# Optimization experiments

Measured on AMD Instinct MI355X. Metric: run time of the kernel, lower is better.

Reference implementation:

```python
import jax, jax.numpy as jnp
import numpy as np

C = 256      # in/out channels
PSI = 4
W = C // PSI          # window width = 64
D = W // 2            # stride = 32
HEADS = 2 * PSI - 1   # 7


def conv_bn_relu(x, Wmat, scale, bias):
    # 1x1 conv (no bias) + inference-mode BN (folded to per-channel scale/bias) + ReLU
    y = jnp.einsum('oc,bcn->bon', Wmat, x)
    return jax.nn.relu(y * scale[:, None] + bias[:, None])


def setup_inputs() -> dict:
    key = jax.random.key(0)
    ks = jax.random.split(key, 16)
    B, N = 4, 2048
    x = jax.random.normal(ks[0], (B, C, N), dtype=jnp.float32)
    Wq = jax.random.normal(ks[1], (C, C), dtype=jnp.float32) / np.sqrt(C)
    Wk = jax.random.normal(ks[2], (C, C), dtype=jnp.float32) / np.sqrt(C)
    Wv = jax.random.normal(ks[3], (C, C), dtype=jnp.float32) / np.sqrt(C)
    sq = jax.random.uniform(ks[4], (C,), dtype=jnp.float32, minval=0.5, maxval=1.5)
    bq = jax.random.normal(ks[5], (C,), dtype=jnp.float32) * 0.1
    sk = jax.random.uniform(ks[6], (C,), dtype=jnp.float32, minval=0.5, maxval=1.5)
    bk = jax.random.normal(ks[7], (C,), dtype=jnp.float32) * 0.1
    sv = jax.random.uniform(ks[8], (C,), dtype=jnp.float32, minval=0.5, maxval=1.5)
    bv = jax.random.normal(ks[9], (C,), dtype=jnp.float32) * 0.1
    Wf = jax.random.normal(ks[10], (C, HEADS * W), dtype=jnp.float32) / np.sqrt(HEADS * W)
    bf = jax.random.normal(ks[11], (C,), dtype=jnp.float32) * 0.1
    sf = jax.random.uniform(ks[12], (C,), dtype=jnp.float32, minval=0.5, maxval=1.5)
    bff = jax.random.normal(ks[13], (C,), dtype=jnp.float32) * 0.1
    return dict(x=x, Wq=Wq, sq=sq, bq=bq, Wk=Wk, sk=sk, bk=bk,
                Wv=Wv, sv=sv, bv=bv, Wf=Wf, bf=bf, sf=sf, bff=bff)


def reference(x, Wq, sq, bq, Wk, sk, bk, Wv, sv, bv, Wf, bf, sf, bff):
    q = conv_bn_relu(x, Wq, sq, bq)   # [B, C, N]
    k = conv_bn_relu(x, Wk, sk, bk)
    v = conv_bn_relu(x, Wv, sv, bv)

    # overlapping channel windows: head m covers channels [m*D, m*D+W)
    win = jnp.arange(HEADS)[:, None] * D + jnp.arange(W)[None, :]  # [HEADS, W]
    qw = q[:, win, :]  # [B, HEADS, W, N]
    kw = k[:, win, :]
    vw = v[:, win, :]

    # a_m = q_m^T k_m over channel window -> [B, HEADS, N, N]
    attn = jnp.einsum('bhwn,bhwm->bhnm', qw, kw)
    attn = jax.nn.softmax(attn, axis=-1)
    # o_m = (a_m v_m^T)^T -> [B, HEADS, W, N]
    o = jnp.einsum('bhnm,bhwm->bhwn', attn, vw)

    B, _, _, N = o.shape
    O = o.reshape(B, HEADS * W, N)  # concat heads along channel dim

    # fusion: 1x1 conv (with bias) + BN + ReLU
    y = jnp.einsum('oc,bcn->bon', Wf, O) + bf[:, None]
    return jax.nn.relu(y * sf[:, None] + bff[:, None])
```

## Files before the change

kernel.cpp:

```cpp
#include <hip/hip_runtime.h>
#include <hip/hip_bf16.h>

typedef __attribute__((ext_vector_type(8))) short bf16x8;
typedef __attribute__((ext_vector_type(4))) float f32x4;

namespace {
constexpr int kC = 256;
constexpr int kN = 2048;
constexpr int kB = 4;
constexpr int kHeads = 7;
constexpr int kOC = kHeads * 64;
constexpr int kSplit = 2;
constexpr int kMChunk = kN / kSplit;
constexpr float kLog2e = 1.44269504f;
}

static __device__ __forceinline__ float bf2f(ushort u) {
    union { unsigned u; float f; } v; v.u = ((unsigned)u) << 16;
    return v.f;
}
static __device__ __forceinline__ unsigned pk_bf16(float a, float b) {
    __hip_bfloat162 h = __float22bfloat162_rn(make_float2(a, b));
    union { __hip_bfloat162 h; unsigned u; } v; v.h = h;
    return v.u;
}
static __device__ __forceinline__ ushort f2bf(float f) {
    return (ushort)(pk_bf16(f, 0.f) & 0xffffu);
}
static __device__ __forceinline__ ushort4 pack4bf(float a, float b, float c, float d) {
    union { ushort4 s; uint2 u; } v;
    v.u.x = pk_bf16(a, b); v.u.y = pk_bf16(c, d);
    return v.s;
}
static __device__ __forceinline__ float fexp2(float x) {
#if __has_builtin(__builtin_amdgcn_exp2f)
    return __builtin_amdgcn_exp2f(x);
#else
    return exp2f(x);
#endif
}
static __device__ __forceinline__ void g2l16(const ushort* g, ushort* l) {
    __builtin_amdgcn_global_load_lds(
        (const __attribute__((address_space(1))) void*)g,
        (__attribute__((address_space(3))) void*)l,
        16, 0, 0);
}

__global__ __launch_bounds__(256) void cast_w_kernel(
    const float* __restrict__ Wq, const float* __restrict__ Wk,
    const float* __restrict__ Wv, const float* __restrict__ Wf,
    ushort* __restrict__ wq, ushort* __restrict__ wk,
    ushort* __restrict__ wv, ushort* __restrict__ wf)
{
    int which = blockIdx.y;
    const float* src = which == 0 ? Wq : which == 1 ? Wk : which == 2 ? Wv : Wf;
    ushort* dst      = which == 0 ? wq : which == 1 ? wk : which == 2 ? wv : wf;
    int n = (which == 3) ? kC * kOC : kC * kC;
    int i = (blockIdx.x * 256 + threadIdx.x) * 4;
    if (i < n) {
        float4 v = *(const float4*)(src + i);
        *(ushort4*)(dst + i) = pack4bf(v.x, v.y, v.z, v.w);
    }
}

__global__ __launch_bounds__(256) void transpose_kernel(
    const float* __restrict__ x, ushort* __restrict__ xT)
{
    const int nt = blockIdx.x, ct = blockIdx.y, b = blockIdx.z;
    __shared__ float T[64][65];
    const int tid = threadIdx.x;
    const float* xb = x + ((size_t)b * kC + ct * 64) * kN + nt * 64;
#pragma unroll
    for (int p = 0; p < 16; ++p) {
        int idx = p * 256 + tid;
        int cc = idx >> 6, nn = idx & 63;
        T[cc][nn] = xb[(size_t)cc * kN + nn];
    }
    __syncthreads();
    ushort* xTb = xT + ((size_t)b * kN + nt * 64) * kC + ct * 64;
#pragma unroll
    for (int p = 0; p < 4; ++p) {
        int nn = p * 16 + (tid >> 4);
        int c4 = (tid & 15) * 4;
        *(ushort4*)&xTb[(size_t)nn * kC + c4] =
            pack4bf(T[c4 + 0][nn], T[c4 + 1][nn], T[c4 + 2][nn], T[c4 + 3][nn]);
    }
}

__global__ __launch_bounds__(256, 2) void qkv_kernel(
    const ushort* __restrict__ xT,
    const ushort* __restrict__ Wqb, const ushort* __restrict__ Wkb, const ushort* __restrict__ Wvb,
    const float* __restrict__ sq, const float* __restrict__ bq,
    const float* __restrict__ sk, const float* __restrict__ bk,
    const float* __restrict__ sv, const float* __restrict__ bv,
    ushort* __restrict__ qT, ushort* __restrict__ kT, ushort* __restrict__ vB)
{
    const int nt  = blockIdx.x;
    const int ot  = blockIdx.y;
    const int b   = blockIdx.z / 3;
    const int mat = blockIdx.z % 3;
    const ushort* Wb = mat == 0 ? Wqb : mat == 1 ? Wkb : Wvb;
    const float* sm = mat == 0 ? sq : mat == 1 ? sk : sv;
    const float* bm = mat == 0 ? bq : mat == 1 ? bk : bv;

    __shared__ __align__(16) ushort lds[4][128 * 64];

    const int tid = threadIdx.x;
    const int lane = tid & 63, wav = tid >> 6;
    const int quad = lane >> 4, l16 = lane & 15;

    const ushort* xTb = xT + ((size_t)b * kN + nt * 128) * kC;
    const ushort* Wt  = Wb + (size_t)(ot * 128) * kC;

    f32x4 acc[8][2];
#pragma unroll
    for (int mt = 0; mt < 8; ++mt)
#pragma unroll
        for (int ntt = 0; ntt < 2; ++ntt)
#pragma unroll
            for (int r = 0; r < 4; ++r) acc[mt][ntt][r] = 0.f;

    const int sa   = lane >> 3;
    const int sblk = (lane & 7) ^ sa;
    auto dmaK = [&](int k0, int buf) {
#pragma unroll
        for (int p = 0; p < 4; ++p) {
            int row = wav * 32 + p * 8 + sa;
            size_t so = (size_t)row * kC + k0 + sblk * 8;
            int dbase = (wav * 32 + p * 8) * 64;
            g2l16(Wt + so,  &lds[buf][dbase]);
            g2l16(xTb + so, &lds[2 + buf][dbase]);
        }
    };

    dmaK(0, 0);
    __syncthreads();

    for (int kt = 0; kt < 4; ++kt) {
        const int cur = kt & 1;
        const bool more = (kt < 3);
        if (more) dmaK((kt + 1) * 64, cur ^ 1);

        const ushort* rowB = (mat < 2) ? lds[cur] : lds[2 + cur];
        const ushort* colB = (mat < 2) ? lds[2 + cur] : lds[cur];
#pragma unroll
        for (int ks = 0; ks < 2; ++ks) {
            bf16x8 bfr[2];
#pragma unroll
            for (int ntt = 0; ntt < 2; ++ntt) {
                int row = wav * 32 + ntt * 16 + l16;
                bfr[ntt] = *(const bf16x8*)&colB[row * 64 + (((ks * 4 + quad) ^ (row & 7)) * 8)];
            }
#pragma unroll
            for (int mt = 0; mt < 8; ++mt) {
                int row = mt * 16 + l16;
                bf16x8 af = *(const bf16x8*)&rowB[row * 64 + (((ks * 4 + quad) ^ (row & 7)) * 8)];
#pragma unroll
                for (int ntt = 0; ntt < 2; ++ntt)
                    acc[mt][ntt] = __builtin_amdgcn_mfma_f32_16x16x32_bf16(
                        af, bfr[ntt], acc[mt][ntt], 0, 0, 0);
            }
        }
        __syncthreads();
    }

    ushort* sT = &lds[0][0];
    const float qs = (mat == 0) ? kLog2e : 1.f;

    if (mat < 2) {
#pragma unroll
        for (int mt = 0; mt < 8; ++mt) {
            float4 sc4 = *(const float4*)&sm[ot * 128 + mt * 16 + quad * 4];
            float4 bi4 = *(const float4*)&bm[ot * 128 + mt * 16 + quad * 4];
#pragma unroll
            for (int ntt = 0; ntt < 2; ++ntt) {
                int nrow = wav * 32 + ntt * 16 + l16;
                float v0 = fmaf(acc[mt][ntt][0], sc4.x, bi4.x) * qs;
                float v1 = fmaf(acc[mt][ntt][1], sc4.y, bi4.y) * qs;
                float v2 = fmaf(acc[mt][ntt][2], sc4.z, bi4.z) * qs;
                float v3 = fmaf(acc[mt][ntt][3], sc4.w, bi4.w) * qs;
                int cb = (mt * 2 + (quad >> 1)) ^ (nrow & 15);
                *(ushort4*)&sT[nrow * 128 + cb * 8 + (quad & 1) * 4] =
                    pack4bf(v0 > 0.f ? v0 : 0.f, v1 > 0.f ? v1 : 0.f,
                            v2 > 0.f ? v2 : 0.f, v3 > 0.f ? v3 : 0.f);
            }
        }
        __syncthreads();
        ushort* out = (mat == 0) ? qT : kT;
#pragma unroll
        for (int p = 0; p < 8; ++p) {
            int idx = p * 256 + tid;
            int row = idx >> 4, blk = idx & 15;
            int4 d = *(const int4*)&sT[row * 128 + ((blk ^ (row & 15)) * 8)];
            *(int4*)&out[((size_t)b * kN + nt * 128 + row) * kC + ot * 128 + blk * 8] = d;
        }
    } else {
#pragma unroll
        for (int ntt = 0; ntt < 2; ++ntt) {
            int orow = wav * 32 + ntt * 16 + l16;
            float sc = sm[ot * 128 + orow], bi = bm[ot * 128 + orow];
#pragma unroll
            for (int mt = 0; mt < 8; ++mt) {
                float v0 = fmaf(acc[mt][ntt][0], sc, bi);
                float v1 = fmaf(acc[mt][ntt][1], sc, bi);
                float v2 = fmaf(acc[mt][ntt][2], sc, bi);
                float v3 = fmaf(acc[mt][ntt][3], sc, bi);
                int cb = (mt * 2 + (quad >> 1)) ^ (orow & 15);
                *(ushort4*)&sT[orow * 128 + cb * 8 + (quad & 1) * 4] =
                    pack4bf(v0 > 0.f ? v0 : 0.f, v1 > 0.f ? v1 : 0.f,
                            v2 > 0.f ? v2 : 0.f, v3 > 0.f ? v3 : 0.f);
            }
        }
        __syncthreads();
#pragma unroll
        for (int p = 0; p < 8; ++p) {
            int idx = p * 256 + tid;
            int row = idx >> 4, blk = idx & 15;
            int4 d = *(const int4*)&sT[row * 128 + ((blk ^ (row & 15)) * 8)];
            *(int4*)&vB[((size_t)b * kC + ot * 128 + row) * kN + nt * 128 + blk * 8] = d;
        }
    }
}

__global__ __launch_bounds__(256, 3) void attn_kernel(
    const ushort* __restrict__ qT, const ushort* __restrict__ kT,
    const ushort* __restrict__ vB,
    ushort* __restrict__ Opart, float* __restrict__ Ls)
{
    const int n0 = blockIdx.x * 128;
    const int h  = blockIdx.y;
    const int s  = blockIdx.z & 1;
    const int b  = blockIdx.z >> 1;
    const int tid = threadIdx.x;
    const int lane = tid & 63, wav = tid >> 6;
    const int quad = lane >> 4, l16 = lane & 15;

    __shared__ __align__(16) ushort sKV[2][8192];
    __shared__ __align__(16) ushort sP[128 * 64];

    const ushort* qTb = qT + (size_t)b * kN * kC;
    const ushort* kTb = kT + (size_t)b * kN * kC;
    const ushort* vbb = vB + ((size_t)b * kC + h * 32) * kN;

    const int arr   = wav >> 1;
    const int rbase = (wav & 1) * 32;

    bf16x8 qf[2][2];
#pragma unroll
    for (int kk = 0; kk < 2; ++kk)
#pragma unroll
        for (int nt2 = 0; nt2 < 2; ++nt2) {
            int ng = n0 + wav * 32 + nt2 * 16 + l16;
            qf[kk][nt2] = *(const bf16x8*)(qTb + (size_t)ng * kC + h * 32 + kk * 32 + quad * 8);
        }

    f32x4 oacc[4][2];
#pragma unroll
    for (int wt = 0; wt < 4; ++wt)
#pragma unroll
        for (int nt2 = 0; nt2 < 2; ++nt2)
#pragma unroll
            for (int r = 0; r < 4; ++r) oacc[wt][nt2][r] = 0.f;
    float li[2] = {0.f, 0.f};

    const int mstart = s * kMChunk;
    const int NIT = kMChunk / 64;

    const int sa   = lane >> 3;
    const int sblk = (lane & 7) ^ sa;
    auto dmaTile = [&](int m0, int buf) {
#pragma unroll
        for (int p = 0; p < 4; ++p) {
            int rl = rbase + p * 8 + sa;
            const ushort* src = (arr == 0)
                ? (kTb + (size_t)(m0 + rl) * kC + h * 32 + sblk * 8)
                : (vbb + (size_t)rl * kN + m0 + sblk * 8);
            g2l16(src, &sKV[buf][arr * 4096 + (rbase + p * 8) * 64]);
        }
    };

    dmaTile(mstart, 0);
    __syncthreads();

    for (int it = 0; it < NIT; ++it) {
        const int cur = it & 1;
        const bool more = (it + 1 < NIT);
        if (more) dmaTile(mstart + (it + 1) * 64, cur ^ 1);

        const ushort* sK = &sKV[cur][0];
        const ushort* sV = &sKV[cur][4096];

        f32x4 sacc[4][2];
#pragma unroll
        for (int mt = 0; mt < 4; ++mt)
#pragma unroll
            for (int nt2 = 0; nt2 < 2; ++nt2)
#pragma unroll
                for (int r = 0; r < 4; ++r) sacc[mt][nt2][r] = 0.f;
#pragma unroll
        for (int kk = 0; kk < 2; ++kk)
#pragma unroll
            for (int mt = 0; mt < 4; ++mt) {
                int row = mt * 16 + l16;
                bf16x8 af = *(const bf16x8*)&sK[row * 64 + (((kk * 4 + quad) ^ (row & 7)) * 8)];
#pragma unroll
                for (int nt2 = 0; nt2 < 2; ++nt2)
                    sacc[mt][nt2] = __builtin_amdgcn_mfma_f32_16x16x32_bf16(
                        af, qf[kk][nt2], sacc[mt][nt2], 0, 0, 0);
            }

#pragma unroll
        for (int nt2 = 0; nt2 < 2; ++nt2) {
            int nrow = wav * 32 + nt2 * 16 + l16;
            float sum = 0.f;
#pragma unroll
            for (int mt = 0; mt < 4; ++mt) {
                float p0 = fexp2(sacc[mt][nt2][0]);
                float p1 = fexp2(sacc[mt][nt2][1]);
                float p2 = fexp2(sacc[mt][nt2][2]);
                float p3 = fexp2(sacc[mt][nt2][3]);
                sum += (p0 + p1) + (p2 + p3);
                int bidx = (mt * 2 + (quad >> 1)) ^ (nrow & 7);
                uint2 pk; pk.x = pk_bf16(p0, p1); pk.y = pk_bf16(p2, p3);
                *(uint2*)&sP[nrow * 64 + bidx * 8 + (quad & 1) * 4] = pk;
            }
            sum += __shfl_xor(sum, 16);
            sum += __shfl_xor(sum, 32);
            li[nt2] += sum;
        }

#pragma unroll
        for (int ks = 0; ks < 2; ++ks) {
            bf16x8 pf[2];
#pragma unroll
            for (int nt2 = 0; nt2 < 2; ++nt2) {
                int nr = wav * 32 + nt2 * 16 + l16;
                pf[nt2] = *(const bf16x8*)&sP[nr * 64 + (((ks * 4 + quad) ^ (nr & 7)) * 8)];
            }
#pragma unroll
            for (int wt = 0; wt < 4; ++wt) {
                int wr = wt * 16 + l16;
                bf16x8 vf = *(const bf16x8*)&sV[wr * 64 + (((ks * 4 + quad) ^ (wr & 7)) * 8)];
#pragma unroll
                for (int nt2 = 0; nt2 < 2; ++nt2)
                    oacc[wt][nt2] = __builtin_amdgcn_mfma_f32_16x16x32_bf16(
                        vf, pf[nt2], oacc[wt][nt2], 0, 0, 0);
            }
        }

        __syncthreads();
    }

#pragma unroll
    for (int nt2 = 0; nt2 < 2; ++nt2) {
        if (quad == 0) {
            int n = n0 + wav * 32 + nt2 * 16 + l16;
            size_t si = ((size_t)(s * kB + b) * kHeads + h) * kN + n;
            Ls[si] = li[nt2];
        }
    }
    ushort* sT = sP;
#pragma unroll
    for (int wt = 0; wt < 4; ++wt)
#pragma unroll
        for (int nt2 = 0; nt2 < 2; ++nt2) {
            float inv = 1.f / li[nt2];
            int nrow = wav * 32 + nt2 * 16 + l16;
            int cb = (wt * 2 + (quad >> 1)) ^ (nrow & 7);
            *(ushort4*)&sT[nrow * 64 + cb * 8 + (quad & 1) * 4] =
                pack4bf(oacc[wt][nt2][0] * inv, oacc[wt][nt2][1] * inv,
                        oacc[wt][nt2][2] * inv, oacc[wt][nt2][3] * inv);
        }
    __syncthreads();
    int rsub = tid >> 3, blk = tid & 7;
#pragma unroll
    for (int p = 0; p < 4; ++p) {
        int row = p * 32 + rsub;
        int4 d = *(const int4*)&sT[row * 64 + ((blk ^ (row & 7)) * 8)];
        *(int4*)&Opart[((size_t)s * kB * kN + (size_t)b * kN + n0 + row) * kOC
                       + h * 64 + blk * 8] = d;
    }
}

__global__ __launch_bounds__(128, 3) void proj_kernel(
    const ushort* __restrict__ Opart, const float* __restrict__ Ls,
    const ushort* __restrict__ Wfb,
    const float* __restrict__ bf_, const float* __restrict__ sf,
    const float* __restrict__ bff, float* __restrict__ out)
{
    const int nt = blockIdx.x;
    const int ot = blockIdx.y;
    const int b  = blockIdx.z;
    __shared__ __align__(16) ushort sA[2][64 * 64];
    __shared__ __align__(16) ushort sB[2][64 * 64];
    const int tid = threadIdx.x;
    const int lane = tid & 63, wav = tid >> 6;
    const int quad = lane >> 4, l16 = lane & 15;

    const ushort* Wt  = Wfb + (size_t)(ot * 64) * kOC;
    const ushort* Op1 = Opart;
    const ushort* Op2 = Opart + (size_t)kB * kN * kOC;
    const size_t soff = (size_t)kB * kHeads * kN;

    f32x4 acc[4][2];
#pragma unroll
    for (int mt = 0; mt < 4; ++mt)
#pragma unroll
        for (int ntt = 0; ntt < 2; ++ntt)
#pragma unroll
            for (int r = 0; r < 4; ++r) acc[mt][ntt][r] = 0.f;

    int4 areg[4], b1reg[4], b2reg[4];
    float w1a[4], w2a[4];

    auto prefetch = [&](int kt) {
        int k0 = kt * 64;
#pragma unroll
        for (int p = 0; p < 4; ++p) {
            int idx = p * 128 + tid, row = idx >> 3, blk = idx & 7;
            areg[p] = *(const int4*)(Wt + (size_t)row * kOC + k0 + blk * 8);
            int n = nt * 64 + row;
            size_t bo = ((size_t)b * kN + n) * kOC + k0 + blk * 8;
            b1reg[p] = *(const int4*)(Op1 + bo);
            b2reg[p] = *(const int4*)(Op2 + bo);
            size_t si = ((size_t)b * kHeads + kt) * kN + n;
            float l1 = Ls[si], l2 = Ls[si + soff];
            float inv = 1.f / (l1 + l2);
            w1a[p] = l1 * inv; w2a[p] = l2 * inv;
        }
    };
    auto stage = [&](int buf) {
#pragma unroll
        for (int p = 0; p < 4; ++p) {
            int idx = p * 128 + tid, row = idx >> 3, blk = idx & 7;
            *(int4*)&sA[buf][row * 64 + ((blk ^ (row & 7)) * 8)] = areg[p];
            union { int4 v; ushort u[8]; } a, c;
            a.v = b1reg[p]; c.v = b2reg[p];
            float rr[8];
#pragma unroll
            for (int j = 0; j < 8; ++j)
                rr[j] = bf2f(a.u[j]) * w1a[p] + bf2f(c.u[j]) * w2a[p];
            int4 o;
            o.x = (int)pk_bf16(rr[0], rr[1]);
            o.y = (int)pk_bf16(rr[2], rr[3]);
            o.z = (int)pk_bf16(rr[4], rr[5]);
            o.w = (int)pk_bf16(rr[6], rr[7]);
            *(int4*)&sB[buf][row * 64 + ((blk ^ (row & 7)) * 8)] = o;
        }
    };

    prefetch(0);
    stage(0);
    __syncthreads();

    for (int kt = 0; kt < 7; ++kt) {
        const int cur = kt & 1;
        const bool more = (kt < 6);
        if (more) prefetch(kt + 1);
#pragma unroll
        for (int ks = 0; ks < 2; ++ks) {
            bf16x8 bfr[2];
#pragma unroll
            for (int ntt = 0; ntt < 2; ++ntt) {
                int row = wav * 32 + ntt * 16 + l16;
                bfr[ntt] = *(const bf16x8*)&sB[cur][row * 64 + (((ks * 4 + quad) ^ (row & 7)) * 8)];
            }
#pragma unroll
            for (int mt = 0; mt < 4; ++mt) {
                int row = mt * 16 + l16;
                bf16x8 af = *(const bf16x8*)&sA[cur][row * 64 + (((ks * 4 + quad) ^ (row & 7)) * 8)];
#pragma unroll
                for (int ntt = 0; ntt < 2; ++ntt)
                    acc[mt][ntt] = __builtin_amdgcn_mfma_f32_16x16x32_bf16(
                        af, bfr[ntt], acc[mt][ntt], 0, 0, 0);
            }
        }
        if (more) stage(cur ^ 1);
        __syncthreads();
    }
#pragma unroll
    for (int mt = 0; mt < 4; ++mt)
#pragma unroll
        for (int r = 0; r < 4; ++r) {
            int o = ot * 64 + mt * 16 + quad * 4 + r;
            float bfv = bf_[o], sfv = sf[o], bffv = bff[o];
#pragma unroll
            for (int ntt = 0; ntt < 2; ++ntt) {
                int n = nt * 64 + wav * 32 + ntt * 16 + l16;
                float y = fmaf(acc[mt][ntt][r] + bfv, sfv, bffv);
                out[((size_t)b * kC + o) * kN + n] = y > 0.f ? y : 0.f;
            }
        }
}

extern "C" void kernel_launch(void* const* d_in, const int* in_sizes, int n_in,
                              void* d_out, int out_size, void* d_ws, size_t ws_size,
                              hipStream_t stream) {
    const float* x   = (const float*)d_in[0];
    const float* Wq  = (const float*)d_in[1];
    const float* sq  = (const float*)d_in[2];
    const float* bq  = (const float*)d_in[3];
    const float* Wk  = (const float*)d_in[4];
    const float* sk  = (const float*)d_in[5];
    const float* bk  = (const float*)d_in[6];
    const float* Wv  = (const float*)d_in[7];
    const float* sv  = (const float*)d_in[8];
    const float* bv  = (const float*)d_in[9];
    const float* Wf  = (const float*)d_in[10];
    const float* bf_ = (const float*)d_in[11];
    const float* sf  = (const float*)d_in[12];
    const float* bff = (const float*)d_in[13];
    float* out = (float*)d_out;

    char* ws = (char*)d_ws;
    ushort* xT  = (ushort*)(ws);
    ushort* Wqb = (ushort*)(ws + 4194304);
    ushort* Wkb = (ushort*)(ws + 4325376);
    ushort* Wvb = (ushort*)(ws + 4456448);
    ushort* Wfb = (ushort*)(ws + 4587520);
    ushort* qT  = (ushort*)(ws + 4816896);
    ushort* kT  = (ushort*)(ws + 9011200);
    ushort* vB  = (ushort*)(ws + 13205504);
    ushort* Opart = (ushort*)(ws + 17399808);
    float*  Ls  = (float*)(ws + 32079872);

    cast_w_kernel<<<dim3(112, 4), 256, 0, stream>>>(Wq, Wk, Wv, Wf, Wqb, Wkb, Wvb, Wfb);
    transpose_kernel<<<dim3(kN / 64, kC / 64, kB), 256, 0, stream>>>(x, xT);
    qkv_kernel<<<dim3(kN / 128, kC / 128, kB * 3), 256, 0, stream>>>(
        xT, Wqb, Wkb, Wvb, sq, bq, sk, bk, sv, bv, qT, kT, vB);
    attn_kernel<<<dim3(kN / 128, kHeads, kB * kSplit), 256, 0, stream>>>(
        qT, kT, vB, Opart, Ls);
    proj_kernel<<<dim3(kN / 64, kC / 64, kB), 128, 0, stream>>>(
        Opart, Ls, Wfb, bf_, sf, bff, out);
}
```

Measured before the change: 168.3 us.

## Split attention keys four ways and combine partial results with fp32 atomics

Raises the key-dimension split of the attention kernel from 2 to 4, doubling the number of attention blocks to improve occupancy across the GPU. Each split now atomically adds its unnormalized fp32 output and row sums into a zeroed workspace, replacing the bf16 partial buffers, the LDS transpose and the weighted two-way merge. The projection kernel then reads the fp32 sums and normalizes by the summed row total. In exchange it adds a memset of about 15 MB and many scalar global atomics with strided addresses, which may contend in L2.

```diff
diff --git a/kernel.cpp b/kernel.cpp
--- a/kernel.cpp
+++ b/kernel.cpp
@@ -10,7 +10,7 @@
 constexpr int kB = 4;
 constexpr int kHeads = 7;
 constexpr int kOC = kHeads * 64;
-constexpr int kSplit = 2;
+constexpr int kSplit = 4;
 constexpr int kMChunk = kN / kSplit;
 constexpr float kLog2e = 1.44269504f;
 }
@@ -23,9 +23,6 @@
     __hip_bfloat162 h = __float22bfloat162_rn(make_float2(a, b));
     union { __hip_bfloat162 h; unsigned u; } v; v.h = h;
     return v.u;
-}
-static __device__ __forceinline__ ushort f2bf(float f) {
-    return (ushort)(pk_bf16(f, 0.f) & 0xffffu);
 }
 static __device__ __forceinline__ ushort4 pack4bf(float a, float b, float c, float d) {
     union { ushort4 s; uint2 u; } v;
@@ -225,12 +222,12 @@
 __global__ __launch_bounds__(256, 3) void attn_kernel(
     const ushort* __restrict__ qT, const ushort* __restrict__ kT,
     const ushort* __restrict__ vB,
-    ushort* __restrict__ Opart, float* __restrict__ Ls)
+    float* __restrict__ Of, float* __restrict__ Lf)
 {
     const int n0 = blockIdx.x * 128;
     const int h  = blockIdx.y;
-    const int s  = blockIdx.z & 1;
-    const int b  = blockIdx.z >> 1;
+    const int s  = blockIdx.z & 3;
+    const int b  = blockIdx.z >> 2;
     const int tid = threadIdx.x;
     const int lane = tid & 63, wav = tid >> 6;
     const int quad = lane >> 4, l16 = lane & 15;
@@ -351,39 +348,23 @@
         __syncthreads();
     }
 
+    float* Ob = Of + ((size_t)b * kN + n0) * kOC + h * 64;
 #pragma unroll
     for (int nt2 = 0; nt2 < 2; ++nt2) {
-        if (quad == 0) {
-            int n = n0 + wav * 32 + nt2 * 16 + l16;
-            size_t si = ((size_t)(s * kB + b) * kHeads + h) * kN + n;
-            Ls[si] = li[nt2];
-        }
-    }
-    ushort* sT = sP;
-#pragma unroll
-    for (int wt = 0; wt < 4; ++wt)
-#pragma unroll
-        for (int nt2 = 0; nt2 < 2; ++nt2) {
-            float inv = 1.f / li[nt2];
-            int nrow = wav * 32 + nt2 * 16 + l16;
-            int cb = (wt * 2 + (quad >> 1)) ^ (nrow & 7);
-            *(ushort4*)&sT[nrow * 64 + cb * 8 + (quad & 1) * 4] =
-                pack4bf(oacc[wt][nt2][0] * inv, oacc[wt][nt2][1] * inv,
-                        oacc[wt][nt2][2] * inv, oacc[wt][nt2][3] * inv);
-        }
-    __syncthreads();
-    int rsub = tid >> 3, blk = tid & 7;
-#pragma unroll
-    for (int p = 0; p < 4; ++p) {
-        int row = p * 32 + rsub;
-        int4 d = *(const int4*)&sT[row * 64 + ((blk ^ (row & 7)) * 8)];
-        *(int4*)&Opart[((size_t)s * kB * kN + (size_t)b * kN + n0 + row) * kOC
-                       + h * 64 + blk * 8] = d;
+        int nl = wav * 32 + nt2 * 16 + l16;
+        if (quad == 0)
+            atomicAdd(Lf + ((size_t)b * kHeads + h) * kN + n0 + nl, li[nt2]);
+#pragma unroll
+        for (int wt = 0; wt < 4; ++wt)
+#pragma unroll
+            for (int r = 0; r < 4; ++r)
+                atomicAdd(Ob + (size_t)nl * kOC + wt * 16 + quad * 4 + r,
+                          oacc[wt][nt2][r]);
     }
 }
 
 __global__ __launch_bounds__(128, 3) void proj_kernel(
-    const ushort* __restrict__ Opart, const float* __restrict__ Ls,
+    const float* __restrict__ Of, const float* __restrict__ Lf,
     const ushort* __restrict__ Wfb,
     const float* __restrict__ bf_, const float* __restrict__ sf,
     const float* __restrict__ bff, float* __restrict__ out)
@@ -397,10 +378,7 @@
     const int lane = tid & 63, wav = tid >> 6;
     const int quad = lane >> 4, l16 = lane & 15;
 
-    const ushort* Wt  = Wfb + (size_t)(ot * 64) * kOC;
-    const ushort* Op1 = Opart;
-    const ushort* Op2 = Opart + (size_t)kB * kN * kOC;
-    const size_t soff = (size_t)kB * kHeads * kN;
+    const ushort* Wt = Wfb + (size_t)(ot * 64) * kOC;
 
     f32x4 acc[4][2];
 #pragma unroll
@@ -410,8 +388,9 @@
 #pragma unroll
             for (int r = 0; r < 4; ++r) acc[mt][ntt][r] = 0.f;
 
-    int4 areg[4], b1reg[4], b2reg[4];
-    float w1a[4], w2a[4];
+    int4 areg[4];
+    float4 o1reg[4], o2reg[4];
+    float winv[4];
 
     auto prefetch = [&](int kt) {
         int k0 = kt * 64;
@@ -420,13 +399,10 @@
             int idx = p * 128 + tid, row = idx >> 3, blk = idx & 7;
             areg[p] = *(const int4*)(Wt + (size_t)row * kOC + k0 + blk * 8);
             int n = nt * 64 + row;
-            size_t bo = ((size_t)b * kN + n) * kOC + k0 + blk * 8;
-            b1reg[p] = *(const int4*)(Op1 + bo);
-            b2reg[p] = *(const int4*)(Op2 + bo);
-            size_t si = ((size_t)b * kHeads + kt) * kN + n;
-            float l1 = Ls[si], l2 = Ls[si + soff];
-            float inv = 1.f / (l1 + l2);
-            w1a[p] = l1 * inv; w2a[p] = l2 * inv;
+            const float* ofp = Of + ((size_t)b * kN + n) * kOC + k0 + blk * 8;
+            o1reg[p] = *(const float4*)(ofp);
+            o2reg[p] = *(const float4*)(ofp + 4);
+            winv[p] = 1.f / Lf[((size_t)b * kHeads + kt) * kN + n];
         }
     };
     auto stage = [&](int buf) {
@@ -434,17 +410,12 @@
         for (int p = 0; p < 4; ++p) {
             int idx = p * 128 + tid, row = idx >> 3, blk = idx & 7;
             *(int4*)&sA[buf][row * 64 + ((blk ^ (row & 7)) * 8)] = areg[p];
-            union { int4 v; ushort u[8]; } a, c;
-            a.v = b1reg[p]; c.v = b2reg[p];
-            float rr[8];
-#pragma unroll
-            for (int j = 0; j < 8; ++j)
-                rr[j] = bf2f(a.u[j]) * w1a[p] + bf2f(c.u[j]) * w2a[p];
+            float iv = winv[p];
             int4 o;
-            o.x = (int)pk_bf16(rr[0], rr[1]);
-            o.y = (int)pk_bf16(rr[2], rr[3]);
-            o.z = (int)pk_bf16(rr[4], rr[5]);
-            o.w = (int)pk_bf16(rr[6], rr[7]);
+            o.x = (int)pk_bf16(o1reg[p].x * iv, o1reg[p].y * iv);
+            o.y = (int)pk_bf16(o1reg[p].z * iv, o1reg[p].w * iv);
+            o.z = (int)pk_bf16(o2reg[p].x * iv, o2reg[p].y * iv);
+            o.w = (int)pk_bf16(o2reg[p].z * iv, o2reg[p].w * iv);
             *(int4*)&sB[buf][row * 64 + ((blk ^ (row & 7)) * 8)] = o;
         }
     };
@@ -521,15 +492,16 @@
     ushort* qT  = (ushort*)(ws + 4816896);
     ushort* kT  = (ushort*)(ws + 9011200);
     ushort* vB  = (ushort*)(ws + 13205504);
-    ushort* Opart = (ushort*)(ws + 17399808);
-    float*  Ls  = (float*)(ws + 32079872);
+    float*  Of  = (float*)(ws + 17399808);
+    float*  Lf  = (float*)(ws + 32079872);
 
     cast_w_kernel<<<dim3(112, 4), 256, 0, stream>>>(Wq, Wk, Wv, Wf, Wqb, Wkb, Wvb, Wfb);
     transpose_kernel<<<dim3(kN / 64, kC / 64, kB), 256, 0, stream>>>(x, xT);
+    hipMemsetAsync(ws + 17399808, 0, 14680064 + 229376, stream);
     qkv_kernel<<<dim3(kN / 128, kC / 128, kB * 3), 256, 0, stream>>>(
         xT, Wqb, Wkb, Wvb, sq, bq, sk, bk, sv, bv, qT, kT, vB);
     attn_kernel<<<dim3(kN / 128, kHeads, kB * kSplit), 256, 0, stream>>>(
-        qT, kT, vB, Opart, Ls);
+        qT, kT, vB, Of, Lf);
     proj_kernel<<<dim3(kN / 64, kC / 64, kB), 128, 0, stream>>>(
-        Opart, Ls, Wfb, bf_, sf, bff, out);
-}
+        Of, Lf, Wfb, bf_, sf, bff, out);
+}
```

Measured after the change: 311.8 us. 1.85x slower.
